# Kernel optimization log

Measured on AMD Instinct MI355X. Metric: run time of the kernel, lower is better.

The kernel has to match this reference:

```python
import jax, jax.numpy as jnp
import numpy as np

N, E, De, Dv = 40000, 8000, 32, 8   # nodes, hyperedges, edge degree, node degree
D, Q, EIG, VOC, NC = 256, 256, 64, 1000, 40  # vertex/edge dim, query dim, eig dim, centrality vocab, classes
LN_EPS = 1e-5


def _linear(x, W, b):
    return x @ W + b


def _layernorm(x, g, b):
    mu = jnp.mean(x, axis=-1, keepdims=True)
    var = jnp.mean(jnp.square(x - mu), axis=-1, keepdims=True)
    return (x - mu) * jax.lax.rsqrt(var + LN_EPS) * g + b


def setup_inputs() -> dict:
    key = jax.random.key(0)
    ks = iter(jax.random.split(key, 64))
    def nrm(shape, s=0.02):
        return (jax.random.normal(next(ks), shape, jnp.float32) * s).astype(jnp.float32)
    inp = {
        'vfeat': jax.random.normal(next(ks), (N, D), jnp.float32),
        'efeat': jax.random.normal(next(ks), (E, D), jnp.float32),
        'eign_vec': jax.random.normal(next(ks), (N, EIG), jnp.float32),
        'feat_v_gcn': jax.random.normal(next(ks), (N, D), jnp.float32),
        'cent1': jax.random.uniform(next(ks), (E, De), jnp.float32),
        'cent2': jax.random.uniform(next(ks), (N, Dv), jnp.float32),
        'cent_idx': jax.random.randint(next(ks), (N,), 0, VOC),
        'uniq_idx': jax.random.randint(next(ks), (N,), 0, VOC),
        'edge2node': jax.random.randint(next(ks), (E, De), 0, N),
        'node2edge': jax.random.randint(next(ks), (N, Dv), 0, E),
        # learned parameters (W: [in, out])
        'W_vtx': nrm((D, D)), 'b_vtx': jnp.zeros((D,), jnp.float32),
        'W_pe': nrm((EIG, D)), 'b_pe': jnp.zeros((D,), jnp.float32),
        'cs_emb': nrm((VOC, D)), 'un_emb': nrm((VOC, D)),
        'W_kv': nrm((D, Q)), 'b_kv': jnp.zeros((Q,), jnp.float32),
        'W_vv': nrm((D, D)), 'b_vv': jnp.zeros((D,), jnp.float32),
        'W_qe': nrm((D, Q)), 'b_qe': jnp.zeros((Q,), jnp.float32),
        'W_ke': nrm((D, Q)), 'b_ke': jnp.zeros((Q,), jnp.float32),
        'W_ve': nrm((D, D)), 'b_ve': jnp.zeros((D,), jnp.float32),
        'W_qv': nrm((D, Q)), 'b_qv': jnp.zeros((Q,), jnp.float32),
        'W_l1': nrm((D, Q)), 'b_l1': jnp.zeros((Q,), jnp.float32),
        'W_l2': nrm((Q, D)), 'b_l2': jnp.zeros((D,), jnp.float32),
        'W_l3': nrm((D, Q)), 'b_l3': jnp.zeros((Q,), jnp.float32),
        'W_l4': nrm((Q, D)), 'b_l4': jnp.zeros((D,), jnp.float32),
        'ln1_g': jnp.ones((D,), jnp.float32), 'ln1_b': jnp.zeros((D,), jnp.float32),
        'ln2_g': jnp.ones((D,), jnp.float32), 'ln2_b': jnp.zeros((D,), jnp.float32),
        'W_cls': nrm((D, NC)), 'b_cls': jnp.zeros((NC,), jnp.float32),
    }
    return inp


def _forward(vfeat, efeat, eign_vec, feat_v_gcn, cent1, cent2,
             W_vtx, b_vtx, W_pe, b_pe, cs_emb, un_emb,
             W_kv, b_kv, W_vv, b_vv, W_qe, b_qe, W_ke, b_ke, W_ve, b_ve, W_qv, b_qv,
             W_l1, b_l1, W_l2, b_l2, W_l3, b_l3, W_l4, b_l4,
             ln1_g, ln1_b, ln2_g, ln2_b, W_cls, b_cls,
             cent_idx, uniq_idx, edge2node, node2edge):
    scale = 1.0 / np.sqrt(float(W_kv.shape[1]))  # 1/sqrt(query_dim)
    # first_layer feature assembly: vtx_lin_1layer + PE + GCN + centrality/uniqueness embeddings
    feat_v = (_linear(vfeat, W_vtx, b_vtx) + _linear(eign_vec, W_pe, b_pe)
              + feat_v_gcn + cs_emb[cent_idx] + un_emb[uniq_idx])
    feat_e = efeat

    # ---- stage 1: hyperedges attend over member nodes ('in' etype) ----
    k_n = _linear(feat_v, W_kv, b_kv)              # [N,Q]
    v_n = _linear(feat_v, W_vv, b_vv)              # [N,D]
    q_e = _linear(feat_e, W_qe, b_qe)              # [E,Q]
    km = k_n[edge2node]                            # [E,De,Q]
    attn = jax.nn.leaky_relu(jnp.einsum('edq,eq->ed', km, q_e), 0.01) * scale
    score = jax.nn.softmax(attn + cent1, axis=1)   # centrality-biased softmax (k-core + clustering)
    h_e = jnp.einsum('ed,edc->ec', score, v_n[edge2node])  # [E,D]
    x_e = _layernorm(h_e + feat_e, ln1_g, ln1_b)
    f_e = _linear(jax.nn.relu(_linear(x_e, W_l1, b_l1)), W_l2, b_l2)
    feat_e = _layernorm(f_e + x_e, ln1_g, ln1_b)

    # ---- stage 2: nodes attend over incident hyperedges ('con' etype) ----
    k_e = _linear(feat_e, W_ke, b_ke)              # [E,Q]
    v_e = _linear(feat_e, W_ve, b_ve)              # [E,D]
    q_v = _linear(feat_v, W_qv, b_qv)              # [N,Q]
    km2 = k_e[node2edge]                           # [N,Dv,Q]
    attn2 = jax.nn.leaky_relu(jnp.einsum('ndq,nq->nd', km2, q_v), 0.01) * scale
    score2 = jax.nn.softmax(attn2 + cent2, axis=1)
    h_v = jnp.einsum('nd,ndc->nc', score2, v_e[node2edge])  # [N,D]
    x_v = _layernorm(h_v + feat_v, ln2_g, ln2_b)
    f_v = _linear(jax.nn.relu(_linear(x_v, W_l3, b_l3)), W_l4, b_l4)
    feat_v = _layernorm(f_v + x_v, ln2_g, ln2_b)

    # last_layer classification head (dropout is identity in eval)
    return _linear(feat_v, W_cls, b_cls)           # [N,NC]


def reference(vfeat, efeat, eign_vec, feat_v_gcn, cent1, cent2,
              cent_idx, uniq_idx, edge2node, node2edge,
              W_vtx, b_vtx, W_pe, b_pe, cs_emb, un_emb,
              W_kv, b_kv, W_vv, b_vv, W_qe, b_qe, W_ke, b_ke, W_ve, b_ve, W_qv, b_qv,
              W_l1, b_l1, W_l2, b_l2, W_l3, b_l3, W_l4, b_l4,
              ln1_g, ln1_b, ln2_g, ln2_b, W_cls, b_cls):
    return _forward(vfeat, efeat, eign_vec, feat_v_gcn, cent1, cent2,
                    W_vtx, b_vtx, W_pe, b_pe, cs_emb, un_emb,
                    W_kv, b_kv, W_vv, b_vv, W_qe, b_qe, W_ke, b_ke, W_ve, b_ve, W_qv, b_qv,
                    W_l1, b_l1, W_l2, b_l2, W_l3, b_l3, W_l4, b_l4,
                    ln1_g, ln1_b, ln2_g, ln2_b, W_cls, b_cls,
                    cent_idx, uniq_idx, edge2node, node2edge)
```

## Files before the change

### kernel.cpp

```cpp
#include <hip/hip_runtime.h>
#include <hip/hip_bf16.h>
#include <cstddef>

#define N_NODES 40000
#define N_EDGES 8000
#define DE 32
#define DV 8
#define DIM 256
#define QDIM 256
#define EIGD 64
#define NCLS 40
#define LN_EPS 1e-5f
#define ATT_SCALE 0.0625f

typedef unsigned short u16;
typedef unsigned int u32;
using i16x8 = __attribute__((ext_vector_type(8))) short;
using f32x4 = __attribute__((ext_vector_type(4))) float;

__device__ inline u16 f2b(float f) {
    union { float f; u32 u; } c; c.f = f;
    u32 u = c.u + 0x7FFF + ((c.u >> 16) & 1);
    return (u16)(u >> 16);
}
__device__ inline float b2f(u16 b) {
    union { u32 u; float f; } c; c.u = (u32)b << 16;
    return c.f;
}

__device__ inline void gload_lds16(const u16* g, u16* l) {
    __builtin_amdgcn_global_load_lds(
        (const __attribute__((address_space(1))) void*)g,
        (__attribute__((address_space(3))) void*)l, 16, 0, 0);
}

#define VMCNT12 asm volatile("s_waitcnt vmcnt(12)" ::: "memory")
#define VMCNT6  asm volatile("s_waitcnt vmcnt(6)" ::: "memory")
#define VMCNT0  asm volatile("s_waitcnt vmcnt(0)" ::: "memory")
#define LGKM0   asm volatile("s_waitcnt lgkmcnt(0)" ::: "memory")
#define SCHED0  __builtin_amdgcn_sched_barrier(0)
#define SBAR    __builtin_amdgcn_s_barrier()

__global__ __launch_bounds__(256) void prep_weights(
    const float* w0, const float* w1, const float* w2, const float* w3,
    const float* w4, const float* w5, const float* w6, const float* w7,
    const float* w8, const float* w9, const float* w10, const float* w11,
    const float* w12, u16* __restrict__ pool)
{
    const float* srcs[13] = {w0,w1,w2,w3,w4,w5,w6,w7,w8,w9,w10,w11,w12};
    const int Ks[13]  = {256,64,256,256,256,256,256,256,256,256,256,256,256};
    const int Nds[13] = {256,256,256,256,256,256,256,256,256,256,256,256,40};
    const int id = blockIdx.z;
    const float* W = srcs[id];
    u16* Wt = pool + (size_t)id * 65536;
    const int K = Ks[id], Nd = Nds[id];
    const int k0 = blockIdx.x * 32, n0 = blockIdx.y * 32;
    if (k0 >= K || n0 >= Nd) return;

    __shared__ float tile[32][33];
    const int x = threadIdx.x & 31, y4 = (threadIdx.x >> 5) * 4;
#pragma unroll
    for (int j = 0; j < 4; j++) {
        int k = k0 + y4 + j;
        tile[y4 + j][x] = (k < K && (n0 + x) < Nd) ? W[(size_t)k * Nd + n0 + x] : 0.f;
    }
    __syncthreads();
#pragma unroll
    for (int j = 0; j < 4; j++) {
        int n = n0 + y4 + j;
        if (n < Nd && (k0 + x) < K)
            Wt[(size_t)n * K + k0 + x] = f2b(tile[x][y4 + j]);
    }
}

#define MST 264
__global__ __launch_bounds__(256, 2) void asm_kvq(
    const float* __restrict__ vfeat, const float* __restrict__ eign,
    const u16* __restrict__ Wt_vtx, const u16* __restrict__ Wt_pe,
    const float* __restrict__ b_vtx, const float* __restrict__ b_pe,
    const float* __restrict__ gcn, const float* __restrict__ emb1,
    const float* __restrict__ emb2, const int* __restrict__ idx1,
    const int* __restrict__ idx2,
    const u16* __restrict__ Wt_kvq, const float* __restrict__ b_kv,
    const float* __restrict__ b_vv, const float* __restrict__ b_qv,
    u16* __restrict__ FVb, u16* __restrict__ KVQn)
{
    __shared__ __align__(16) u16 Asm[2][64 * 32];
    __shared__ __align__(16) u16 Bsm[2][256 * 32];
    __shared__ __align__(16) u16 Msm[64 * MST];
    const int t = threadIdx.x;
    const int lane = t & 63, w = t >> 6;
    const int row0 = blockIdx.x * 64;

    const int srow = lane >> 2;
    const int sblk = ((lane & 3) ^ ((lane >> 3) & 3)) * 8;
    const int fr = lane & 15, h = lane >> 4;
    const int rsw = (fr >> 1) & 3;

    f32x4 acc[4][4] = {};
    float4 fA[2][2];

    auto p1_issueB = [&](int kt) {
        const int buf = kt & 1;
        const int k0 = kt << 5;
        const bool tail = (k0 >= 256);
#pragma unroll
        for (int i = 0; i < 4; i++) {
            const int r = w * 64 + i * 16;
            const u16* gp = tail ? Wt_pe + (size_t)(r + srow) * 64 + (k0 - 256) + sblk
                                 : Wt_vtx + (size_t)(r + srow) * 256 + k0 + sblk;
            gload_lds16(gp, &Bsm[buf][r * 32]);
        }
    };
    auto p1_loadA = [&](int kt) {
        const int k0 = kt << 5;
        const bool tail = (k0 >= 256);
        const float* ap = tail
            ? eign + (size_t)(row0 + w * 16 + srow) * 64 + (k0 - 256) + sblk
            : vfeat + (size_t)(row0 + w * 16 + srow) * 256 + k0 + sblk;
        fA[kt & 1][0] = *(const float4*)ap;
        fA[kt & 1][1] = *(const float4*)(ap + 4);
    };
    auto p1_write = [&](int kt) {
        const int buf = kt & 1;
        float4 f0 = fA[buf][0], f1 = fA[buf][1];
        i16x8 v;
        v[0] = (short)f2b(f0.x); v[1] = (short)f2b(f0.y);
        v[2] = (short)f2b(f0.z); v[3] = (short)f2b(f0.w);
        v[4] = (short)f2b(f1.x); v[5] = (short)f2b(f1.y);
        v[6] = (short)f2b(f1.z); v[7] = (short)f2b(f1.w);
        *(i16x8*)&Asm[buf][(w * 16 + srow) * 32 + (lane & 3) * 8] = v;
    };

    p1_loadA(0); p1_issueB(0); p1_loadA(1); p1_write(0);
#pragma unroll
    for (int kt = 0; kt < 10; ++kt) {
        const int buf = kt & 1;
        if (kt + 1 < 10) p1_issueB(kt + 1);
        if (kt + 2 < 10) p1_loadA(kt + 2);
        if (kt + 1 < 10) p1_write(kt + 1);
        else { VMCNT0; }
        LGKM0;
        SBAR;

        i16x8 af[4], bfr[4];
#pragma unroll
        for (int m = 0; m < 4; m++)
            af[m] = *(const i16x8*)&Asm[buf][(m * 16 + fr) * 32 + (h ^ rsw) * 8];
#pragma unroll
        for (int n = 0; n < 4; n++)
            bfr[n] = *(const i16x8*)&Bsm[buf][(w * 64 + n * 16 + fr) * 32 + (h ^ rsw) * 8];
        LGKM0;
        SCHED0;
        SBAR;

#pragma unroll
        for (int m = 0; m < 4; m++)
#pragma unroll
            for (int n = 0; n < 4; n++)
                acc[m][n] = __builtin_amdgcn_mfma_f32_16x16x32_bf16(
                    af[m], bfr[n], acc[m][n], 0, 0, 0);
    }

#pragma unroll
    for (int m = 0; m < 4; m++)
#pragma unroll
        for (int j = 0; j < 4; j++) {
            const int row = m * 16 + h * 4 + j;
#pragma unroll
            for (int n = 0; n < 4; n++) {
                const int col = w * 64 + n * 16 + fr;
                float v = acc[m][n][j] + b_vtx[col] + b_pe[col];
                Msm[row * MST + col] = f2b(v);
                acc[m][n][j] = 0.f;
            }
        }
    __syncthreads();

    const float4* gcn4 = (const float4*)gcn;
    const float4* e1_4 = (const float4*)emb1;
    const float4* e2_4 = (const float4*)emb2;
    ushort4* FVb4 = (ushort4*)FVb;
#pragma unroll 4
    for (int it = 0; it < 16; ++it) {
        const int T = t + it * 256;
        const int row = T >> 6, cg = T & 63;
        const int grow = row0 + row;
        const int i1 = idx1[grow], i2 = idx2[grow];
        ushort4 mv = *(const ushort4*)&Msm[row * MST + cg * 4];
        float4 gv = gcn4[(size_t)grow * 64 + cg];
        float4 e1 = e1_4[(size_t)i1 * 64 + cg];
        float4 e2 = e2_4[(size_t)i2 * 64 + cg];
        ushort4 o;
        o.x = f2b(b2f(mv.x) + gv.x + e1.x + e2.x);
        o.y = f2b(b2f(mv.y) + gv.y + e1.y + e2.y);
        o.z = f2b(b2f(mv.z) + gv.z + e1.z + e2.z);
        o.w = f2b(b2f(mv.w) + gv.w + e1.w + e2.w);
        FVb4[(size_t)grow * 64 + cg] = o;
        *(ushort4*)&Msm[row * MST + cg * 4] = o;
    }
    __syncthreads();

    auto p2_issueB = [&](int buf, int kt, const u16* Wb) {
#pragma unroll
        for (int i = 0; i < 4; i++) {
            const int r = w * 64 + i * 16;
            gload_lds16(Wb + (size_t)(r + srow) * 256 + (kt << 5) + sblk,
                        &Bsm[buf][r * 32]);
        }
    };
    p2_issueB(0, 0, Wt_kvq);
    VMCNT0; SBAR;
#pragma unroll 1
    for (int c = 0; c < 3; ++c) {
        const u16* Wb = Wt_kvq + (size_t)c * 65536;
        const float* bc = (c == 0) ? b_kv : ((c == 1) ? b_vv : b_qv);
#pragma unroll
        for (int m = 0; m < 4; m++)
#pragma unroll
            for (int n = 0; n < 4; n++)
                acc[m][n] = f32x4{0.f, 0.f, 0.f, 0.f};
#pragma unroll
        for (int kt = 0; kt < 8; ++kt) {
            const int buf = kt & 1;
            if (kt < 7) p2_issueB(buf ^ 1, kt + 1, Wb);
            else if (c < 2) p2_issueB(0, 0, Wb + 65536);

            i16x8 af[4], bfr[4];
#pragma unroll
            for (int m = 0; m < 4; m++)
                af[m] = *(const i16x8*)&Msm[(m * 16 + fr) * MST + (kt << 5) + h * 8];
#pragma unroll
            for (int n = 0; n < 4; n++)
                bfr[n] = *(const i16x8*)&Bsm[buf][(w * 64 + n * 16 + fr) * 32 + (h ^ rsw) * 8];
            LGKM0;
            SCHED0;
#pragma unroll
            for (int m = 0; m < 4; m++)
#pragma unroll
                for (int n = 0; n < 4; n++)
                    acc[m][n] = __builtin_amdgcn_mfma_f32_16x16x32_bf16(
                        af[m], bfr[n], acc[m][n], 0, 0, 0);
            if (kt < 7) { VMCNT0; SBAR; }
        }
#pragma unroll
        for (int m = 0; m < 4; m++)
#pragma unroll
            for (int j = 0; j < 4; j++) {
                const int grow = row0 + m * 16 + h * 4 + j;
#pragma unroll
                for (int n = 0; n < 4; n++) {
                    const int gcol = w * 64 + n * 16 + fr;
                    KVQn[(size_t)grow * 768 + c * 256 + gcol] =
                        f2b(acc[m][n][j] + bc[gcol]);
                }
            }
        if (c < 2) { VMCNT0; SBAR; }
    }
}

template <int EPI, int AMODE, int NT>
__global__ __launch_bounds__(256, 2) void gemmN(
    const void* __restrict__ Av, const u16* __restrict__ Wt,
    const float* __restrict__ bias0, const float* __restrict__ bias1,
    const float* __restrict__ bias2,
    void* __restrict__ Cv, int Nd)
{
    __shared__ u16 Asm[3][64 * 64];
    __shared__ u16 Bsm[3][128 * 64];
    const int t = threadIdx.x;
    const int lane = t & 63, w = t >> 6;
    const int wr = w >> 1, wc = w & 1;
    const int row0 = blockIdx.y * 64, col0 = blockIdx.x * 128;

    f32x4 acc[2][4] = {};

    const int srow = lane >> 3;
    const int sblk = ((lane & 7) ^ srow) * 8;
    const int fr = lane & 15, h = lane >> 4;
    const int lsw = fr & 7;

    float4 farA[2][2][2];

    auto stage_load = [&](int kt) {
        const int buf = kt % 3;
        const int k0 = kt << 6;
        if constexpr (AMODE == 0) {
#pragma unroll
            for (int i = 0; i < 2; i++) {
                const int r = w * 16 + i * 8;
                gload_lds16((const u16*)Av + (size_t)(row0 + r + srow) * 256 + k0 + sblk,
                            &Asm[buf][r * 64]);
            }
        } else {
#pragma unroll
            for (int i = 0; i < 2; i++) {
                const int r = w * 16 + i * 8;
                const float* ap = (const float*)Av + (size_t)(row0 + r + srow) * 256 + k0 + sblk;
                farA[kt & 1][i][0] = *(const float4*)ap;
                farA[kt & 1][i][1] = *(const float4*)(ap + 4);
            }
        }
#pragma unroll
        for (int i = 0; i < 4; i++) {
            const int r = w * 32 + i * 8;
            int ng = col0 + r + srow; if (ng > Nd - 1) ng = Nd - 1;
            gload_lds16(Wt + (size_t)ng * 256 + k0 + sblk, &Bsm[buf][r * 64]);
        }
    };
    auto stage_write = [&](int kt) {
        const int buf = kt % 3;
#pragma unroll
        for (int i = 0; i < 2; i++) {
            const int r = w * 16 + i * 8;
            float4 f0 = farA[kt & 1][i][0], f1 = farA[kt & 1][i][1];
            i16x8 v;
            v[0] = (short)f2b(f0.x); v[1] = (short)f2b(f0.y);
            v[2] = (short)f2b(f0.z); v[3] = (short)f2b(f0.w);
            v[4] = (short)f2b(f1.x); v[5] = (short)f2b(f1.y);
            v[6] = (short)f2b(f1.z); v[7] = (short)f2b(f1.w);
            *(i16x8*)&Asm[buf][(r + srow) * 64 + (lane & 7) * 8] = v;
        }
    };

    stage_load(0);
    if (NT > 1) stage_load(1);
    if constexpr (AMODE != 0) stage_write(0);

#pragma unroll
    for (int kt = 0; kt < NT; ++kt) {
        const int buf = kt % 3;
        if (kt + 2 < NT) stage_load(kt + 2);
        if constexpr (AMODE != 0) {
            if (kt + 1 < NT) stage_write(kt + 1);
            else { VMCNT0; }
        } else {
            if (kt + 2 < NT) { VMCNT12; }
            else if (kt + 1 < NT) { VMCNT6; }
            else { VMCNT0; }
        }
        LGKM0;
        SBAR;

        i16x8 af[2][2], bfr[2][4];
#pragma unroll
        for (int kk = 0; kk < 2; kk++) {
#pragma unroll
            for (int m = 0; m < 2; m++)
                af[kk][m] = *(const i16x8*)&Asm[buf][(wr * 32 + m * 16 + fr) * 64 +
                                                    ((kk * 4 + h) ^ lsw) * 8];
#pragma unroll
            for (int n = 0; n < 4; n++)
                bfr[kk][n] = *(const i16x8*)&Bsm[buf][(wc * 64 + n * 16 + fr) * 64 +
                                                     ((kk * 4 + h) ^ lsw) * 8];
        }
        LGKM0;
        SCHED0;
        SBAR;

#pragma unroll
        for (int kk = 0; kk < 2; kk++)
#pragma unroll
            for (int m = 0; m < 2; m++)
#pragma unroll
                for (int n = 0; n < 4; n++)
                    acc[m][n] = __builtin_amdgcn_mfma_f32_16x16x32_bf16(
                        af[kk][m], bfr[kk][n], acc[m][n], 0, 0, 0);
    }

    const int seg = (int)(blockIdx.x >> 1);
    const float* bp = (seg == 0) ? bias0 : ((seg == 1) ? bias1 : bias2);
#pragma unroll
    for (int m = 0; m < 2; m++) {
#pragma unroll
        for (int j = 0; j < 4; j++) {
            const int grow = row0 + wr * 32 + m * 16 + h * 4 + j;
#pragma unroll
            for (int n = 0; n < 4; n++) {
                const int gcol = col0 + wc * 64 + n * 16 + fr;
                if (EPI == 4 && gcol >= Nd) continue;
                float v = acc[m][n][j] + bp[gcol & 255];
                if constexpr (EPI == 1) v = fmaxf(v, 0.f);
                if constexpr (EPI == 4)
                    ((float*)Cv)[(size_t)grow * Nd + gcol] = v;
                else
                    ((u16*)Cv)[(size_t)grow * Nd + gcol] = f2b(v);
            }
        }
    }
}

template <int TAIL>
__global__ __launch_bounds__(256, 2) void ffn_fused(
    const u16* __restrict__ X, const u16* __restrict__ Wt1,
    const float* __restrict__ b1, const u16* __restrict__ Wt2,
    const float* __restrict__ b2, const float* __restrict__ lng,
    const float* __restrict__ lnb, const u16* __restrict__ WtT,
    const float* __restrict__ bT0, const float* __restrict__ bT1,
    void* __restrict__ outp)
{
    __shared__ __align__(16) u16 Asm[2][64 * 32];
    __shared__ __align__(16) u16 Bsm[2][256 * 32];
    __shared__ __align__(16) u16 Msm[64 * MST];
    const int t = threadIdx.x;
    const int lane = t & 63, w = t >> 6;
    const int row0 = blockIdx.x * 64;

    const int srow = lane >> 2;
    const int sblk = ((lane & 3) ^ ((lane >> 3) & 3)) * 8;
    const int fr = lane & 15, h = lane >> 4;
    const int rsw = (fr >> 1) & 3;

    f32x4 acc[4][4] = {};

    auto stageA = [&](int buf, int kt) {
        gload_lds16(X + (size_t)(row0 + w * 16 + srow) * 256 + (kt << 5) + sblk,
                    &Asm[buf][(w * 16) * 32]);
    };
    auto stageB = [&](int buf, int kt, const u16* W) {
#pragma unroll
        for (int i = 0; i < 4; i++) {
            const int r = w * 64 + i * 16;
            gload_lds16(W + (size_t)(r + srow) * 256 + (kt << 5) + sblk,
                        &Bsm[buf][r * 32]);
        }
    };

    stageA(0, 0); stageB(0, 0, Wt1);
    VMCNT0; SBAR;
#pragma unroll
    for (int kt = 0; kt < 8; ++kt) {
        const int buf = kt & 1;
        if (kt < 7) { stageA(buf ^ 1, kt + 1); stageB(buf ^ 1, kt + 1, Wt1); }
        else        { stageB(0, 0, Wt2); }

        i16x8 af[4], bfr[4];
#pragma unroll
        for (int m = 0; m < 4; m++)
            af[m] = *(const i16x8*)&Asm[buf][(m * 16 + fr) * 32 + (h ^ rsw) * 8];
#pragma unroll
        for (int n = 0; n < 4; n++)
            bfr[n] = *(const i16x8*)&Bsm[buf][(w * 64 + n * 16 + fr) * 32 + (h ^ rsw) * 8];
        LGKM0;
        SCHED0;
#pragma unroll
        for (int m = 0; m < 4; m++)
#pragma unroll
            for (int n = 0; n < 4; n++)
                acc[m][n] = __builtin_amdgcn_mfma_f32_16x16x32_bf16(
                    af[m], bfr[n], acc[m][n], 0, 0, 0);
        if (kt < 7) { VMCNT0; SBAR; }
    }
    {
        float b1v[4];
#pragma unroll
        for (int n = 0; n < 4; n++) b1v[n] = b1[w * 64 + n * 16 + fr];
#pragma unroll
        for (int m = 0; m < 4; m++)
#pragma unroll
            for (int j = 0; j < 4; j++) {
                const int row = m * 16 + h * 4 + j;
#pragma unroll
                for (int n = 0; n < 4; n++) {
                    const int col = w * 64 + n * 16 + fr;
                    float v = fmaxf(acc[m][n][j] + b1v[n], 0.f);
                    Msm[row * MST + col] = f2b(v);
                    acc[m][n][j] = 0.f;
                }
            }
    }
    __syncthreads();

#pragma unroll
    for (int kt = 0; kt < 8; ++kt) {
        const int buf = kt & 1;
        if (kt < 7) stageB(buf ^ 1, kt + 1, Wt2);
        else if (TAIL == 0) stageB(0, 0, WtT);

        i16x8 af[4], bfr[4];
#pragma unroll
        for (int m = 0; m < 4; m++)
            af[m] = *(const i16x8*)&Msm[(m * 16 + fr) * MST + (kt << 5) + h * 8];
#pragma unroll
        for (int n = 0; n < 4; n++)
            bfr[n] = *(const i16x8*)&Bsm[buf][(w * 64 + n * 16 + fr) * 32 + (h ^ rsw) * 8];
        LGKM0;
        SCHED0;
#pragma unroll
        for (int m = 0; m < 4; m++)
#pragma unroll
            for (int n = 0; n < 4; n++)
                acc[m][n] = __builtin_amdgcn_mfma_f32_16x16x32_bf16(
                    af[m], bfr[n], acc[m][n], 0, 0, 0);
        if (kt < 7) { VMCNT0; SBAR; }
    }
    {
        float* redS = (float*)&Asm[0][0];
        float* redQ = redS + 256;
#pragma unroll
        for (int m = 0; m < 4; m++) {
#pragma unroll
            for (int j = 0; j < 4; j++) {
                const int grow = row0 + m * 16 + h * 4 + j;
                float s = 0.f, q = 0.f;
#pragma unroll
                for (int n = 0; n < 4; n++) {
                    const int gcol = w * 64 + n * 16 + fr;
                    float v = acc[m][n][j] + b2[gcol] +
                              b2f(X[(size_t)grow * 256 + gcol]);
                    acc[m][n][j] = v;
                    s += v; q += v * v;
                }
#pragma unroll
                for (int off = 1; off < 16; off <<= 1) {
                    s += __shfl_xor(s, off, 64);
                    q += __shfl_xor(q, off, 64);
                }
                if (fr == 0) {
                    redS[(m * 16 + h * 4 + j) * 4 + w] = s;
                    redQ[(m * 16 + h * 4 + j) * 4 + w] = q;
                }
            }
        }
        __syncthreads();
#pragma unroll
        for (int m = 0; m < 4; m++) {
#pragma unroll
            for (int j = 0; j < 4; j++) {
                const int r = m * 16 + h * 4 + j;
                float4 s4 = *(const float4*)&redS[r * 4];
                float4 q4 = *(const float4*)&redQ[r * 4];
                float mu = (s4.x + s4.y + s4.z + s4.w) * (1.f / DIM);
                float var = (q4.x + q4.y + q4.z + q4.w) * (1.f / DIM) - mu * mu;
                float rr = rsqrtf(var + LN_EPS);
#pragma unroll
                for (int n = 0; n < 4; n++) {
                    const int gcol = w * 64 + n * 16 + fr;
                    float y = (acc[m][n][j] - mu) * rr * lng[gcol] + lnb[gcol];
                    acc[m][n][j] = y;
                }
            }
        }
        __syncthreads();
#pragma unroll
        for (int m = 0; m < 4; m++)
#pragma unroll
            for (int j = 0; j < 4; j++) {
                const int row = m * 16 + h * 4 + j;
#pragma unroll
                for (int n = 0; n < 4; n++)
                    Msm[row * MST + (w * 64 + n * 16 + fr)] = f2b(acc[m][n][j]);
            }
    }
    __syncthreads();

    if constexpr (TAIL == 0) {
        u16* KVe = (u16*)outp;
#pragma unroll 1
        for (int half = 0; half < 2; half++) {
            const u16* Wb = WtT + (size_t)half * 65536;
            const float* bT = half ? bT1 : bT0;
#pragma unroll
            for (int m = 0; m < 4; m++)
#pragma unroll
                for (int n = 0; n < 4; n++)
                    acc[m][n] = f32x4{0.f, 0.f, 0.f, 0.f};
#pragma unroll
            for (int kt = 0; kt < 8; ++kt) {
                const int buf = kt & 1;
                if (kt < 7) stageB(buf ^ 1, kt + 1, Wb);
                else if (half == 0) stageB(0, 0, WtT + 65536);

                i16x8 af[4], bfr[4];
#pragma unroll
                for (int m = 0; m < 4; m++)
                    af[m] = *(const i16x8*)&Msm[(m * 16 + fr) * MST + (kt << 5) + h * 8];
#pragma unroll
                for (int n = 0; n < 4; n++)
                    bfr[n] = *(const i16x8*)&Bsm[buf][(w * 64 + n * 16 + fr) * 32 + (h ^ rsw) * 8];
                LGKM0;
                SCHED0;
#pragma unroll
                for (int m = 0; m < 4; m++)
#pragma unroll
                    for (int n = 0; n < 4; n++)
                        acc[m][n] = __builtin_amdgcn_mfma_f32_16x16x32_bf16(
                            af[m], bfr[n], acc[m][n], 0, 0, 0);
                if (kt < 7) { VMCNT0; SBAR; }
            }
#pragma unroll
            for (int m = 0; m < 4; m++)
#pragma unroll
                for (int j = 0; j < 4; j++) {
                    const int grow = row0 + m * 16 + h * 4 + j;
#pragma unroll
                    for (int n = 0; n < 4; n++) {
                        const int gcol = w * 64 + n * 16 + fr;
                        KVe[(size_t)grow * 512 + half * 256 + gcol] =
                            f2b(acc[m][n][j] + bT[gcol]);
                    }
                }
            if (half == 0) { VMCNT0; SBAR; }
        }
    } else {
        float* out = (float*)outp;
        f32x4 acc3[3] = {};
#pragma unroll
        for (int kk = 0; kk < 8; kk++) {
            i16x8 af = *(const i16x8*)&Msm[(w * 16 + fr) * MST + kk * 32 + h * 8];
#pragma unroll
            for (int n = 0; n < 3; n++) {
                int br = n * 16 + fr; if (br > NCLS - 1) br = NCLS - 1;
                i16x8 bfr = *(const i16x8*)(WtT + (size_t)br * 256 + kk * 32 + h * 8);
                acc3[n] = __builtin_amdgcn_mfma_f32_16x16x32_bf16(af, bfr, acc3[n], 0, 0, 0);
            }
        }
#pragma unroll
        for (int n = 0; n < 3; n++) {
            const int gcol = n * 16 + fr;
            if (gcol >= NCLS) continue;
#pragma unroll
            for (int j = 0; j < 4; j++) {
                const int grow = row0 + w * 16 + h * 4 + j;
                out[(size_t)grow * NCLS + gcol] = acc3[n][j] + bT0[gcol];
            }
        }
    }
}

__global__ __launch_bounds__(256) void edge_attn(
    const u16* __restrict__ KVQn, const u16* __restrict__ QE,
    const float* __restrict__ efeat,
    const int* __restrict__ e2n, const float* __restrict__ cent1,
    const float* __restrict__ g, const float* __restrict__ bb,
    u16* __restrict__ XE)
{
    const int lane = threadIdx.x & 63, w = threadIdx.x >> 6;
    const int e = blockIdx.x * 4 + w;
    const int c4 = lane * 4;

    ushort4 q4 = *(const ushort4*)&QE[(size_t)e * QDIM + c4];
    const float q0 = b2f(q4.x), q1 = b2f(q4.y), q2 = b2f(q4.z), q3 = b2f(q4.w);

    int4 rv[8];
#pragma unroll
    for (int i = 0; i < 8; i++)
        rv[i] = *(const int4*)&e2n[(size_t)e * DE + i * 4];
    int rows[DE];
#pragma unroll
    for (int i = 0; i < 8; i++) {
        rows[i * 4 + 0] = rv[i].x; rows[i * 4 + 1] = rv[i].y;
        rows[i * 4 + 2] = rv[i].z; rows[i * 4 + 3] = rv[i].w;
    }

    float p[DE];
#pragma unroll
    for (int g0 = 0; g0 < DE; g0 += 16) {
        ushort4 k4[16];
#pragma unroll
        for (int j = 0; j < 16; j++)
            k4[j] = *(const ushort4*)&KVQn[(size_t)rows[g0 + j] * 768 + c4];
#pragma unroll
        for (int j = 0; j < 16; j++)
            p[g0 + j] = q0 * b2f(k4[j].x) + q1 * b2f(k4[j].y)
                      + q2 * b2f(k4[j].z) + q3 * b2f(k4[j].w);
    }
#pragma unroll
    for (int off = 32; off; off >>= 1)
#pragma unroll
        for (int d = 0; d < DE; d++)
            p[d] += __shfl_xor(p[d], off, 64);

    float4 cv[8];
#pragma unroll
    for (int i = 0; i < 8; i++)
        cv[i] = *(const float4*)&cent1[(size_t)e * DE + i * 4];
    float cent[DE];
#pragma unroll
    for (int i = 0; i < 8; i++) {
        cent[i * 4 + 0] = cv[i].x; cent[i * 4 + 1] = cv[i].y;
        cent[i * 4 + 2] = cv[i].z; cent[i * 4 + 3] = cv[i].w;
    }
#pragma unroll
    for (int d = 0; d < DE; d++)
        p[d] = (p[d] > 0.f ? p[d] : 0.01f * p[d]) * ATT_SCALE + cent[d];

    float mx = p[0];
#pragma unroll
    for (int d = 1; d < DE; d++) mx = fmaxf(mx, p[d]);
    float s = 0.f;
#pragma unroll
    for (int d = 0; d < DE; d++) { p[d] = __expf(p[d] - mx); s += p[d]; }
    const float inv = 1.f / s;
#pragma unroll
    for (int d = 0; d < DE; d++) p[d] *= inv;

    float a0 = 0.f, a1 = 0.f, a2 = 0.f, a3 = 0.f;
#pragma unroll
    for (int g0 = 0; g0 < DE; g0 += 16) {
        ushort4 v4[16];
#pragma unroll
        for (int j = 0; j < 16; j++)
            v4[j] = *(const ushort4*)&KVQn[(size_t)rows[g0 + j] * 768 + 256 + c4];
#pragma unroll
        for (int j = 0; j < 16; j++) {
            const float sd = p[g0 + j];
            a0 = fmaf(sd, b2f(v4[j].x), a0); a1 = fmaf(sd, b2f(v4[j].y), a1);
            a2 = fmaf(sd, b2f(v4[j].z), a2); a3 = fmaf(sd, b2f(v4[j].w), a3);
        }
    }
    float4 ef = *(const float4*)&efeat[(size_t)e * DIM + c4];
    float x0 = a0 + ef.x, x1 = a1 + ef.y, x2 = a2 + ef.z, x3 = a3 + ef.w;

    float mu = x0 + x1 + x2 + x3;
#pragma unroll
    for (int off = 32; off; off >>= 1) mu += __shfl_xor(mu, off, 64);
    mu *= (1.f / DIM);
    float d0 = x0 - mu, d1 = x1 - mu, d2 = x2 - mu, d3 = x3 - mu;
    float var = d0 * d0 + d1 * d1 + d2 * d2 + d3 * d3;
#pragma unroll
    for (int off = 32; off; off >>= 1) var += __shfl_xor(var, off, 64);
    var *= (1.f / DIM);
    float r = rsqrtf(var + LN_EPS);
    float4 gv = *(const float4*)&g[c4];
    float4 bv = *(const float4*)&bb[c4];
    ushort4 o;
    o.x = f2b(d0 * r * gv.x + bv.x); o.y = f2b(d1 * r * gv.y + bv.y);
    o.z = f2b(d2 * r * gv.z + bv.z); o.w = f2b(d3 * r * gv.w + bv.w);
    *(ushort4*)&XE[(size_t)e * DIM + c4] = o;
}

__global__ __launch_bounds__(256) void node_attn(
    const u16* __restrict__ KVe, const u16* __restrict__ KVQn,
    const u16* __restrict__ FV,
    const int* __restrict__ n2e, const float* __restrict__ cent2,
    const float* __restrict__ g, const float* __restrict__ bb,
    u16* __restrict__ XV)
{
    const int lane = threadIdx.x & 63, w = threadIdx.x >> 6;
    const int na = blockIdx.x * 8 + w * 2, nb = na + 1;
    const int c4 = lane * 4;

    ushort4 qa4 = *(const ushort4*)&KVQn[(size_t)na * 768 + 512 + c4];
    ushort4 qb4 = *(const ushort4*)&KVQn[(size_t)nb * 768 + 512 + c4];
    const float qa0 = b2f(qa4.x), qa1 = b2f(qa4.y), qa2 = b2f(qa4.z), qa3 = b2f(qa4.w);
    const float qb0 = b2f(qb4.x), qb1 = b2f(qb4.y), qb2 = b2f(qb4.z), qb3 = b2f(qb4.w);

    int4 r0 = *(const int4*)&n2e[(size_t)na * DV];
    int4 r1 = *(const int4*)&n2e[(size_t)na * DV + 4];
    int4 r2 = *(const int4*)&n2e[(size_t)nb * DV];
    int4 r3 = *(const int4*)&n2e[(size_t)nb * DV + 4];
    int rA[8] = {r0.x, r0.y, r0.z, r0.w, r1.x, r1.y, r1.z, r1.w};
    int rB[8] = {r2.x, r2.y, r2.z, r2.w, r3.x, r3.y, r3.z, r3.w};

    ushort4 kA[8], vA[8], kB[8], vB[8];
#pragma unroll
    for (int d = 0; d < DV; d++) {
        const u16* b = KVe + (size_t)rA[d] * 512 + c4;
        kA[d] = *(const ushort4*)b; vA[d] = *(const ushort4*)(b + 256);
    }
#pragma unroll
    for (int d = 0; d < DV; d++) {
        const u16* b = KVe + (size_t)rB[d] * 512 + c4;
        kB[d] = *(const ushort4*)b; vB[d] = *(const ushort4*)(b + 256);
    }

    float pA[8], pB[8];
#pragma unroll
    for (int d = 0; d < DV; d++) {
        pA[d] = qa0 * b2f(kA[d].x) + qa1 * b2f(kA[d].y)
              + qa2 * b2f(kA[d].z) + qa3 * b2f(kA[d].w);
        pB[d] = qb0 * b2f(kB[d].x) + qb1 * b2f(kB[d].y)
              + qb2 * b2f(kB[d].z) + qb3 * b2f(kB[d].w);
    }
#pragma unroll
    for (int off = 32; off; off >>= 1) {
#pragma unroll
        for (int d = 0; d < DV; d++) {
            pA[d] += __shfl_xor(pA[d], off, 64);
            pB[d] += __shfl_xor(pB[d], off, 64);
        }
    }
    float4 cA0 = *(const float4*)&cent2[(size_t)na * DV];
    float4 cA1 = *(const float4*)&cent2[(size_t)na * DV + 4];
    float4 cB0 = *(const float4*)&cent2[(size_t)nb * DV];
    float4 cB1 = *(const float4*)&cent2[(size_t)nb * DV + 4];
    float cA[8] = {cA0.x, cA0.y, cA0.z, cA0.w, cA1.x, cA1.y, cA1.z, cA1.w};
    float cB[8] = {cB0.x, cB0.y, cB0.z, cB0.w, cB1.x, cB1.y, cB1.z, cB1.w};
#pragma unroll
    for (int d = 0; d < DV; d++) {
        pA[d] = (pA[d] > 0.f ? pA[d] : 0.01f * pA[d]) * ATT_SCALE + cA[d];
        pB[d] = (pB[d] > 0.f ? pB[d] : 0.01f * pB[d]) * ATT_SCALE + cB[d];
    }
    float mA = pA[0], mB = pB[0];
#pragma unroll
    for (int d = 1; d < DV; d++) { mA = fmaxf(mA, pA[d]); mB = fmaxf(mB, pB[d]); }
    float sA = 0.f, sB = 0.f;
#pragma unroll
    for (int d = 0; d < DV; d++) {
        pA[d] = __expf(pA[d] - mA); sA += pA[d];
        pB[d] = __expf(pB[d] - mB); sB += pB[d];
    }
    const float iA = 1.f / sA, iB = 1.f / sB;

    float a0 = 0.f, a1 = 0.f, a2 = 0.f, a3 = 0.f;
    float b0 = 0.f, b1 = 0.f, b2 = 0.f, b3 = 0.f;
#pragma unroll
    for (int d = 0; d < DV; d++) {
        const float sa = pA[d] * iA, sb = pB[d] * iB;
        a0 = fmaf(sa, b2f(vA[d].x), a0); a1 = fmaf(sa, b2f(vA[d].y), a1);
        a2 = fmaf(sa, b2f(vA[d].z), a2); a3 = fmaf(sa, b2f(vA[d].w), a3);
        b0 = fmaf(sb, b2f(vB[d].x), b0); b1 = fmaf(sb, b2f(vB[d].y), b1);
        b2 = fmaf(sb, b2f(vB[d].z), b2); b3 = fmaf(sb, b2f(vB[d].w), b3);
    }
    ushort4 fa = *(const ushort4*)&FV[(size_t)na * DIM + c4];
    ushort4 fb = *(const ushort4*)&FV[(size_t)nb * DIM + c4];
    float xa0 = a0 + b2f(fa.x), xa1 = a1 + b2f(fa.y);
    float xa2 = a2 + b2f(fa.z), xa3 = a3 + b2f(fa.w);
    float xb0 = b0 + b2f(fb.x), xb1 = b1 + b2f(fb.y);
    float xb2 = b2 + b2f(fb.z), xb3 = b3 + b2f(fb.w);

    float muA = xa0 + xa1 + xa2 + xa3, muB = xb0 + xb1 + xb2 + xb3;
#pragma unroll
    for (int off = 32; off; off >>= 1) {
        muA += __shfl_xor(muA, off, 64);
        muB += __shfl_xor(muB, off, 64);
    }
    muA *= (1.f / DIM); muB *= (1.f / DIM);
    float da0 = xa0 - muA, da1 = xa1 - muA, da2 = xa2 - muA, da3 = xa3 - muA;
    float db0 = xb0 - muB, db1 = xb1 - muB, db2 = xb2 - muB, db3 = xb3 - muB;
    float vA_ = da0 * da0 + da1 * da1 + da2 * da2 + da3 * da3;
    float vB_ = db0 * db0 + db1 * db1 + db2 * db2 + db3 * db3;
#pragma unroll
    for (int off = 32; off; off >>= 1) {
        vA_ += __shfl_xor(vA_, off, 64);
        vB_ += __shfl_xor(vB_, off, 64);
    }
    const float rA_ = rsqrtf(vA_ * (1.f / DIM) + LN_EPS);
    const float rB_ = rsqrtf(vB_ * (1.f / DIM) + LN_EPS);
    float4 gv = *(const float4*)&g[c4];
    float4 bv = *(const float4*)&bb[c4];
    ushort4 oa, ob;
    oa.x = f2b(da0 * rA_ * gv.x + bv.x); oa.y = f2b(da1 * rA_ * gv.y + bv.y);
    oa.z = f2b(da2 * rA_ * gv.z + bv.z); oa.w = f2b(da3 * rA_ * gv.w + bv.w);
    ob.x = f2b(db0 * rB_ * gv.x + bv.x); ob.y = f2b(db1 * rB_ * gv.y + bv.y);
    ob.z = f2b(db2 * rB_ * gv.z + bv.z); ob.w = f2b(db3 * rB_ * gv.w + bv.w);
    *(ushort4*)&XV[(size_t)na * DIM + c4] = oa;
    *(ushort4*)&XV[(size_t)nb * DIM + c4] = ob;
}

extern "C" void kernel_launch(void* const* d_in, const int* in_sizes, int n_in,
                              void* d_out, int out_size, void* d_ws, size_t ws_size,
                              hipStream_t stream)
{
    const float* vfeat  = (const float*)d_in[0];
    const float* efeat  = (const float*)d_in[1];
    const float* eign   = (const float*)d_in[2];
    const float* gcn    = (const float*)d_in[3];
    const float* cent1  = (const float*)d_in[4];
    const float* cent2  = (const float*)d_in[5];
    const int*   cidx   = (const int*)d_in[6];
    const int*   uidx   = (const int*)d_in[7];
    const int*   e2n    = (const int*)d_in[8];
    const int*   n2e    = (const int*)d_in[9];
    const float* W_vtx  = (const float*)d_in[10]; const float* b_vtx = (const float*)d_in[11];
    const float* W_pe   = (const float*)d_in[12]; const float* b_pe  = (const float*)d_in[13];
    const float* cs_emb = (const float*)d_in[14]; const float* un_emb= (const float*)d_in[15];
    const float* W_kv   = (const float*)d_in[16]; const float* b_kv  = (const float*)d_in[17];
    const float* W_vv   = (const float*)d_in[18]; const float* b_vv  = (const float*)d_in[19];
    const float* W_qe   = (const float*)d_in[20]; const float* b_qe  = (const float*)d_in[21];
    const float* W_ke   = (const float*)d_in[22]; const float* b_ke  = (const float*)d_in[23];
    const float* W_ve   = (const float*)d_in[24]; const float* b_ve  = (const float*)d_in[25];
    const float* W_qv   = (const float*)d_in[26]; const float* b_qv  = (const float*)d_in[27];
    const float* W_l1   = (const float*)d_in[28]; const float* b_l1  = (const float*)d_in[29];
    const float* W_l2   = (const float*)d_in[30]; const float* b_l2  = (const float*)d_in[31];
    const float* W_l3   = (const float*)d_in[32]; const float* b_l3  = (const float*)d_in[33];
    const float* W_l4   = (const float*)d_in[34]; const float* b_l4  = (const float*)d_in[35];
    const float* ln1_g  = (const float*)d_in[36]; const float* ln1_b = (const float*)d_in[37];
    const float* ln2_g  = (const float*)d_in[38]; const float* ln2_b = (const float*)d_in[39];
    const float* W_cls  = (const float*)d_in[40]; const float* b_cls = (const float*)d_in[41];
    float* out = (float*)d_out;

    const size_t NE = (size_t)N_NODES * DIM;
    const size_t EE = (size_t)N_EDGES * DIM;
    u16* ws = (u16*)d_ws;
    u16* FVb  = ws;
    u16* KVQn = FVb + NE;
    u16* B2   = KVQn + 3 * NE;
    u16* QEb  = B2 + NE;
    u16* XE   = QEb + EE;
    u16* KVe  = XE + EE;
    u16* Wp   = KVe + 2 * EE;
    u16* Wt_vtx = Wp +  0 * 65536;
    u16* Wt_pe  = Wp +  1 * 65536;
    u16* Wt_kvq = Wp +  2 * 65536;
    u16* Wt_qe  = Wp +  5 * 65536;
    u16* Wt_kve = Wp +  6 * 65536;
    u16* Wt_l1  = Wp +  8 * 65536;
    u16* Wt_l2  = Wp +  9 * 65536;
    u16* Wt_l3  = Wp + 10 * 65536;
    u16* Wt_l4  = Wp + 11 * 65536;
    u16* Wt_cls = Wp + 12 * 65536;

    const dim3 blk(256);
    const dim3 gW(8, 8, 13);
    const dim3 gQE(2, N_EDGES / 64);

    prep_weights<<<gW, blk, 0, stream>>>(
        W_vtx, W_pe, W_kv, W_vv, W_qv, W_qe, W_ke, W_ve,
        W_l1, W_l2, W_l3, W_l4, W_cls, Wp);

    asm_kvq<<<N_NODES / 64, blk, 0, stream>>>(
        vfeat, eign, Wt_vtx, Wt_pe, b_vtx, b_pe,
        gcn, cs_emb, un_emb, cidx, uidx,
        Wt_kvq, b_kv, b_vv, b_qv, FVb, KVQn);

    gemmN<0, 1, 4><<<gQE, blk, 0, stream>>>(efeat, Wt_qe,
        b_qe, b_qe, b_qe, QEb, 256);
    edge_attn<<<N_EDGES / 4, blk, 0, stream>>>(KVQn, QEb, efeat, e2n, cent1,
        ln1_g, ln1_b, XE);
    ffn_fused<0><<<N_EDGES / 64, blk, 0, stream>>>(XE, Wt_l1, b_l1,
        Wt_l2, b_l2, ln1_g, ln1_b, Wt_kve, b_ke, b_ve, KVe);

    node_attn<<<N_NODES / 8, blk, 0, stream>>>(KVe, KVQn, FVb, n2e, cent2,
        ln2_g, ln2_b, B2);
    ffn_fused<1><<<N_NODES / 64, blk, 0, stream>>>(B2, Wt_l3, b_l3,
        Wt_l4, b_l4, ln2_g, ln2_b, Wt_cls, b_cls, nullptr, out);
}
```

Before: 237.7 us.

## Drop LDS staging buffer in asm_kvq and stream FV tiles from global memory

Removes the 33 KB Msm shared-memory tile from asm_kvq. The feature-assembly epilogue now adds gcn and embedding rows straight from the MFMA accumulators and writes FVb to global memory. The second GEMM stages A tiles of FVb back through the double-buffered Asm via global-to-LDS loads. Launch bounds rise to 4 blocks per CU to exploit the lower LDS footprint. The cost is uncoalesced scalar gathers in the epilogue and re-reading FVb from global/L2, and it relies on VMCNT0 plus a barrier making the block's own FVb writes visible to its later loads.

```diff
diff --git a/kernel.cpp b/kernel.cpp
--- a/kernel.cpp
+++ b/kernel.cpp
@@ -73,8 +73,7 @@
     }
 }
 
-#define MST 264
-__global__ __launch_bounds__(256, 2) void asm_kvq(
+__global__ __launch_bounds__(256, 4) void asm_kvq(
     const float* __restrict__ vfeat, const float* __restrict__ eign,
     const u16* __restrict__ Wt_vtx, const u16* __restrict__ Wt_pe,
     const float* __restrict__ b_vtx, const float* __restrict__ b_pe,
@@ -87,7 +86,6 @@
 {
     __shared__ __align__(16) u16 Asm[2][64 * 32];
     __shared__ __align__(16) u16 Bsm[2][256 * 32];
-    __shared__ __align__(16) u16 Msm[64 * MST];
     const int t = threadIdx.x;
     const int lane = t & 63, w = t >> 6;
     const int row0 = blockIdx.x * 64;
@@ -163,45 +161,31 @@
     }
 
 #pragma unroll
-    for (int m = 0; m < 4; m++)
+    for (int m = 0; m < 4; m++) {
 #pragma unroll
         for (int j = 0; j < 4; j++) {
-            const int row = m * 16 + h * 4 + j;
+            const int grow = row0 + m * 16 + h * 4 + j;
+            const int i1 = idx1[grow], i2 = idx2[grow];
 #pragma unroll
             for (int n = 0; n < 4; n++) {
-                const int col = w * 64 + n * 16 + fr;
-                float v = acc[m][n][j] + b_vtx[col] + b_pe[col];
-                Msm[row * MST + col] = f2b(v);
+                const int gcol = w * 64 + n * 16 + fr;
+                float v = acc[m][n][j] + b_vtx[gcol] + b_pe[gcol];
+                v += gcn[(size_t)grow * 256 + gcol];
+                v += emb1[(size_t)i1 * 256 + gcol];
+                v += emb2[(size_t)i2 * 256 + gcol];
+                FVb[(size_t)grow * 256 + gcol] = f2b(v);
                 acc[m][n][j] = 0.f;
             }
         }
-    __syncthreads();
-
-    const float4* gcn4 = (const float4*)gcn;
-    const float4* e1_4 = (const float4*)emb1;
-    const float4* e2_4 = (const float4*)emb2;
-    ushort4* FVb4 = (ushort4*)FVb;
-#pragma unroll 4
-    for (int it = 0; it < 16; ++it) {
-        const int T = t + it * 256;
-        const int row = T >> 6, cg = T & 63;
-        const int grow = row0 + row;
-        const int i1 = idx1[grow], i2 = idx2[grow];
-        ushort4 mv = *(const ushort4*)&Msm[row * MST + cg * 4];
-        float4 gv = gcn4[(size_t)grow * 64 + cg];
-        float4 e1 = e1_4[(size_t)i1 * 64 + cg];
-        float4 e2 = e2_4[(size_t)i2 * 64 + cg];
-        ushort4 o;
-        o.x = f2b(b2f(mv.x) + gv.x + e1.x + e2.x);
-        o.y = f2b(b2f(mv.y) + gv.y + e1.y + e2.y);
-        o.z = f2b(b2f(mv.z) + gv.z + e1.z + e2.z);
-        o.w = f2b(b2f(mv.w) + gv.w + e1.w + e2.w);
-        FVb4[(size_t)grow * 64 + cg] = o;
-        *(ushort4*)&Msm[row * MST + cg * 4] = o;
-    }
-    __syncthreads();
-
-    auto p2_issueB = [&](int buf, int kt, const u16* Wb) {
+    }
+    VMCNT0;
+    SBAR;
+
+    auto p2_stageA = [&](int buf, int kt) {
+        gload_lds16(FVb + (size_t)(row0 + w * 16 + srow) * 256 + (kt << 5) + sblk,
+                    &Asm[buf][(w * 16) * 32]);
+    };
+    auto p2_stageB = [&](int buf, int kt, const u16* Wb) {
 #pragma unroll
         for (int i = 0; i < 4; i++) {
             const int r = w * 64 + i * 16;
@@ -209,27 +193,22 @@
                         &Bsm[buf][r * 32]);
         }
     };
-    p2_issueB(0, 0, Wt_kvq);
+    p2_stageA(0, 0); p2_stageB(0, 0, Wt_kvq);
     VMCNT0; SBAR;
 #pragma unroll 1
     for (int c = 0; c < 3; ++c) {
         const u16* Wb = Wt_kvq + (size_t)c * 65536;
         const float* bc = (c == 0) ? b_kv : ((c == 1) ? b_vv : b_qv);
 #pragma unroll
-        for (int m = 0; m < 4; m++)
-#pragma unroll
-            for (int n = 0; n < 4; n++)
-                acc[m][n] = f32x4{0.f, 0.f, 0.f, 0.f};
-#pragma unroll
         for (int kt = 0; kt < 8; ++kt) {
             const int buf = kt & 1;
-            if (kt < 7) p2_issueB(buf ^ 1, kt + 1, Wb);
-            else if (c < 2) p2_issueB(0, 0, Wb + 65536);
+            if (kt < 7) { p2_stageA(buf ^ 1, kt + 1); p2_stageB(buf ^ 1, kt + 1, Wb); }
+            else if (c < 2) { p2_stageA(0, 0); p2_stageB(0, 0, Wb + 65536); }
 
             i16x8 af[4], bfr[4];
 #pragma unroll
             for (int m = 0; m < 4; m++)
-                af[m] = *(const i16x8*)&Msm[(m * 16 + fr) * MST + (kt << 5) + h * 8];
+                af[m] = *(const i16x8*)&Asm[buf][(m * 16 + fr) * 32 + (h ^ rsw) * 8];
 #pragma unroll
             for (int n = 0; n < 4; n++)
                 bfr[n] = *(const i16x8*)&Bsm[buf][(w * 64 + n * 16 + fr) * 32 + (h ^ rsw) * 8];
@@ -253,6 +232,7 @@
                     const int gcol = w * 64 + n * 16 + fr;
                     KVQn[(size_t)grow * 768 + c * 256 + gcol] =
                         f2b(acc[m][n][j] + bc[gcol]);
+                    acc[m][n][j] = 0.f;
                 }
             }
         if (c < 2) { VMCNT0; SBAR; }
@@ -390,6 +370,7 @@
     }
 }
 
+#define MST 264
 template <int TAIL>
 __global__ __launch_bounds__(256, 2) void ffn_fused(
     const u16* __restrict__ X, const u16* __restrict__ Wt1,
```

New measurement: 337.0 us. 41.8% more time.

## Read weight fragments directly from global memory instead of staging through LDS

Applied to the files above, without the earlier changes.

Removes the double-buffered LDS staging of the weight (B) tiles in the fused assemble/KVQ and FFN kernels. Each wave now loads its B fragments straight from global/L2, which also drops the per-k-step barriers and vmcnt waits. The LDS saving is used to raise launch bounds from two to three blocks per CU. The cost is uncoalesced 16-byte global loads of weights on the MFMA critical path with no prefetch, plus higher register pressure from separate accumulators.

```diff
diff --git a/kernel.cpp b/kernel.cpp
--- a/kernel.cpp
+++ b/kernel.cpp
@@ -74,7 +74,7 @@
 }
 
 #define MST 264
-__global__ __launch_bounds__(256, 2) void asm_kvq(
+__global__ __launch_bounds__(256, 3) void asm_kvq(
     const float* __restrict__ vfeat, const float* __restrict__ eign,
     const u16* __restrict__ Wt_vtx, const u16* __restrict__ Wt_pe,
     const float* __restrict__ b_vtx, const float* __restrict__ b_pe,
@@ -86,7 +86,6 @@
     u16* __restrict__ FVb, u16* __restrict__ KVQn)
 {
     __shared__ __align__(16) u16 Asm[2][64 * 32];
-    __shared__ __align__(16) u16 Bsm[2][256 * 32];
     __shared__ __align__(16) u16 Msm[64 * MST];
     const int t = threadIdx.x;
     const int lane = t & 63, w = t >> 6;
@@ -100,18 +99,6 @@
     f32x4 acc[4][4] = {};
     float4 fA[2][2];
 
-    auto p1_issueB = [&](int kt) {
-        const int buf = kt & 1;
-        const int k0 = kt << 5;
-        const bool tail = (k0 >= 256);
-#pragma unroll
-        for (int i = 0; i < 4; i++) {
-            const int r = w * 64 + i * 16;
-            const u16* gp = tail ? Wt_pe + (size_t)(r + srow) * 64 + (k0 - 256) + sblk
-                                 : Wt_vtx + (size_t)(r + srow) * 256 + k0 + sblk;
-            gload_lds16(gp, &Bsm[buf][r * 32]);
-        }
-    };
     auto p1_loadA = [&](int kt) {
         const int k0 = kt << 5;
         const bool tail = (k0 >= 256);
@@ -132,11 +119,10 @@
         *(i16x8*)&Asm[buf][(w * 16 + srow) * 32 + (lane & 3) * 8] = v;
     };
 
-    p1_loadA(0); p1_issueB(0); p1_loadA(1); p1_write(0);
+    p1_loadA(0); p1_loadA(1); p1_write(0);
 #pragma unroll
     for (int kt = 0; kt < 10; ++kt) {
         const int buf = kt & 1;
-        if (kt + 1 < 10) p1_issueB(kt + 1);
         if (kt + 2 < 10) p1_loadA(kt + 2);
         if (kt + 1 < 10) p1_write(kt + 1);
         else { VMCNT0; }
@@ -147,9 +133,16 @@
 #pragma unroll
         for (int m = 0; m < 4; m++)
             af[m] = *(const i16x8*)&Asm[buf][(m * 16 + fr) * 32 + (h ^ rsw) * 8];
-#pragma unroll
-        for (int n = 0; n < 4; n++)
-            bfr[n] = *(const i16x8*)&Bsm[buf][(w * 64 + n * 16 + fr) * 32 + (h ^ rsw) * 8];
+        {
+            const bool tail = (kt >= 8);
+#pragma unroll
+            for (int n = 0; n < 4; n++) {
+                const int br = w * 64 + n * 16 + fr;
+                bfr[n] = tail
+                    ? *(const i16x8*)(Wt_pe + (size_t)br * 64 + ((kt - 8) << 5) + h * 8)
+                    : *(const i16x8*)(Wt_vtx + (size_t)br * 256 + (kt << 5) + h * 8);
+            }
+        }
         LGKM0;
         SCHED0;
         SBAR;
@@ -172,7 +165,6 @@
                 const int col = w * 64 + n * 16 + fr;
                 float v = acc[m][n][j] + b_vtx[col] + b_pe[col];
                 Msm[row * MST + col] = f2b(v);
-                acc[m][n][j] = 0.f;
             }
         }
     __syncthreads();
@@ -201,47 +193,27 @@
     }
     __syncthreads();
 
-    auto p2_issueB = [&](int buf, int kt, const u16* Wb) {
-#pragma unroll
-        for (int i = 0; i < 4; i++) {
-            const int r = w * 64 + i * 16;
-            gload_lds16(Wb + (size_t)(r + srow) * 256 + (kt << 5) + sblk,
-                        &Bsm[buf][r * 32]);
-        }
-    };
-    p2_issueB(0, 0, Wt_kvq);
-    VMCNT0; SBAR;
 #pragma unroll 1
     for (int c = 0; c < 3; ++c) {
         const u16* Wb = Wt_kvq + (size_t)c * 65536;
         const float* bc = (c == 0) ? b_kv : ((c == 1) ? b_vv : b_qv);
-#pragma unroll
-        for (int m = 0; m < 4; m++)
-#pragma unroll
-            for (int n = 0; n < 4; n++)
-                acc[m][n] = f32x4{0.f, 0.f, 0.f, 0.f};
+        f32x4 a2[4][4] = {};
 #pragma unroll
         for (int kt = 0; kt < 8; ++kt) {
-            const int buf = kt & 1;
-            if (kt < 7) p2_issueB(buf ^ 1, kt + 1, Wb);
-            else if (c < 2) p2_issueB(0, 0, Wb + 65536);
-
             i16x8 af[4], bfr[4];
 #pragma unroll
             for (int m = 0; m < 4; m++)
                 af[m] = *(const i16x8*)&Msm[(m * 16 + fr) * MST + (kt << 5) + h * 8];
 #pragma unroll
             for (int n = 0; n < 4; n++)
-                bfr[n] = *(const i16x8*)&Bsm[buf][(w * 64 + n * 16 + fr) * 32 + (h ^ rsw) * 8];
-            LGKM0;
-            SCHED0;
+                bfr[n] = *(const i16x8*)(Wb + (size_t)(w * 64 + n * 16 + fr) * 256 +
+                                         (kt << 5) + h * 8);
 #pragma unroll
             for (int m = 0; m < 4; m++)
 #pragma unroll
                 for (int n = 0; n < 4; n++)
-                    acc[m][n] = __builtin_amdgcn_mfma_f32_16x16x32_bf16(
-                        af[m], bfr[n], acc[m][n], 0, 0, 0);
-            if (kt < 7) { VMCNT0; SBAR; }
+                    a2[m][n] = __builtin_amdgcn_mfma_f32_16x16x32_bf16(
+                        af[m], bfr[n], a2[m][n], 0, 0, 0);
         }
 #pragma unroll
         for (int m = 0; m < 4; m++)
@@ -252,10 +224,9 @@
                 for (int n = 0; n < 4; n++) {
                     const int gcol = w * 64 + n * 16 + fr;
                     KVQn[(size_t)grow * 768 + c * 256 + gcol] =
-                        f2b(acc[m][n][j] + bc[gcol]);
+                        f2b(a2[m][n][j] + bc[gcol]);
                 }
             }
-        if (c < 2) { VMCNT0; SBAR; }
     }
 }
 
@@ -391,7 +362,7 @@
 }
 
 template <int TAIL>
-__global__ __launch_bounds__(256, 2) void ffn_fused(
+__global__ __launch_bounds__(256, 3) void ffn_fused(
     const u16* __restrict__ X, const u16* __restrict__ Wt1,
     const float* __restrict__ b1, const u16* __restrict__ Wt2,
     const float* __restrict__ b2, const float* __restrict__ lng,
@@ -400,7 +371,6 @@
     void* __restrict__ outp)
 {
     __shared__ __align__(16) u16 Asm[2][64 * 32];
-    __shared__ __align__(16) u16 Bsm[2][256 * 32];
     __shared__ __align__(16) u16 Msm[64 * MST];
     const int t = threadIdx.x;
     const int lane = t & 63, w = t >> 6;
@@ -417,22 +387,13 @@
         gload_lds16(X + (size_t)(row0 + w * 16 + srow) * 256 + (kt << 5) + sblk,
                     &Asm[buf][(w * 16) * 32]);
     };
-    auto stageB = [&](int buf, int kt, const u16* W) {
-#pragma unroll
-        for (int i = 0; i < 4; i++) {
-            const int r = w * 64 + i * 16;
-            gload_lds16(W + (size_t)(r + srow) * 256 + (kt << 5) + sblk,
-                        &Bsm[buf][r * 32]);
-        }
-    };
-
-    stageA(0, 0); stageB(0, 0, Wt1);
+
+    stageA(0, 0);
     VMCNT0; SBAR;
 #pragma unroll
     for (int kt = 0; kt < 8; ++kt) {
         const int buf = kt & 1;
-        if (kt < 7) { stageA(buf ^ 1, kt + 1); stageB(buf ^ 1, kt + 1, Wt1); }
-        else        { stageB(0, 0, Wt2); }
+        if (kt < 7) stageA(buf ^ 1, kt + 1);
 
         i16x8 af[4], bfr[4];
 #pragma unroll
@@ -440,7 +401,8 @@
             af[m] = *(const i16x8*)&Asm[buf][(m * 16 + fr) * 32 + (h ^ rsw) * 8];
 #pragma unroll
         for (int n = 0; n < 4; n++)
-            bfr[n] = *(const i16x8*)&Bsm[buf][(w * 64 + n * 16 + fr) * 32 + (h ^ rsw) * 8];
+            bfr[n] = *(const i16x8*)(Wt1 + (size_t)(w * 64 + n * 16 + fr) * 256 +
+                                     (kt << 5) + h * 8);
         LGKM0;
         SCHED0;
 #pragma unroll
@@ -473,26 +435,20 @@
 
 #pragma unroll
     for (int kt = 0; kt < 8; ++kt) {
-        const int buf = kt & 1;
-        if (kt < 7) stageB(buf ^ 1, kt + 1, Wt2);
-        else if (TAIL == 0) stageB(0, 0, WtT);
-
         i16x8 af[4], bfr[4];
 #pragma unroll
         for (int m = 0; m < 4; m++)
             af[m] = *(const i16x8*)&Msm[(m * 16 + fr) * MST + (kt << 5) + h * 8];
 #pragma unroll
         for (int n = 0; n < 4; n++)
-            bfr[n] = *(const i16x8*)&Bsm[buf][(w * 64 + n * 16 + fr) * 32 + (h ^ rsw) * 8];
-        LGKM0;
-        SCHED0;
+            bfr[n] = *(const i16x8*)(Wt2 + (size_t)(w * 64 + n * 16 + fr) * 256 +
+                                     (kt << 5) + h * 8);
 #pragma unroll
         for (int m = 0; m < 4; m++)
 #pragma unroll
             for (int n = 0; n < 4; n++)
                 acc[m][n] = __builtin_amdgcn_mfma_f32_16x16x32_bf16(
                     af[m], bfr[n], acc[m][n], 0, 0, 0);
-        if (kt < 7) { VMCNT0; SBAR; }
     }
     {
         float* redS = (float*)&Asm[0][0];
@@ -560,33 +516,23 @@
         for (int half = 0; half < 2; half++) {
             const u16* Wb = WtT + (size_t)half * 65536;
             const float* bT = half ? bT1 : bT0;
-#pragma unroll
-            for (int m = 0; m < 4; m++)
-#pragma unroll
-                for (int n = 0; n < 4; n++)
-                    acc[m][n] = f32x4{0.f, 0.f, 0.f, 0.f};
+            f32x4 a2[4][4] = {};
 #pragma unroll
             for (int kt = 0; kt < 8; ++kt) {
-                const int buf = kt & 1;
-                if (kt < 7) stageB(buf ^ 1, kt + 1, Wb);
-                else if (half == 0) stageB(0, 0, WtT + 65536);
-
                 i16x8 af[4], bfr[4];
 #pragma unroll
                 for (int m = 0; m < 4; m++)
                     af[m] = *(const i16x8*)&Msm[(m * 16 + fr) * MST + (kt << 5) + h * 8];
 #pragma unroll
                 for (int n = 0; n < 4; n++)
-                    bfr[n] = *(const i16x8*)&Bsm[buf][(w * 64 + n * 16 + fr) * 32 + (h ^ rsw) * 8];
-                LGKM0;
-                SCHED0;
+                    bfr[n] = *(const i16x8*)(Wb + (size_t)(w * 64 + n * 16 + fr) * 256 +
+                                             (kt << 5) + h * 8);
 #pragma unroll
                 for (int m = 0; m < 4; m++)
 #pragma unroll
                     for (int n = 0; n < 4; n++)
-                        acc[m][n] = __builtin_amdgcn_mfma_f32_16x16x32_bf16(
-                            af[m], bfr[n], acc[m][n], 0, 0, 0);
-                if (kt < 7) { VMCNT0; SBAR; }
+                        a2[m][n] = __builtin_amdgcn_mfma_f32_16x16x32_bf16(
+                            af[m], bfr[n], a2[m][n], 0, 0, 0);
             }
 #pragma unroll
             for (int m = 0; m < 4; m++)
@@ -597,10 +543,9 @@
                     for (int n = 0; n < 4; n++) {
                         const int gcol = w * 64 + n * 16 + fr;
                         KVe[(size_t)grow * 512 + half * 256 + gcol] =
-                            f2b(acc[m][n][j] + bT[gcol]);
+                            f2b(a2[m][n][j] + bT[gcol]);
                     }
                 }
-            if (half == 0) { VMCNT0; SBAR; }
         }
     } else {
         float* out = (float*)outp;
```

Result: slower. 311.2 us (+30.9%).
